# Optimization experiments

Measured on AMD Instinct MI355X. Metric: run time of the kernel, lower is better.

Reference implementation:

```python
import jax, jax.numpy as jnp
import numpy as np

NF, NLOC, NNEI = 4, 2048, 64
EMBED, PAIR_DIM, H = 128, 64, 8
HD = EMBED // H
EPS = 1e-5

def _ln(x, g, b):
    m = x.mean(-1, keepdims=True)
    v = ((x - m) ** 2).mean(-1, keepdims=True)
    return (x - m) * jax.lax.rsqrt(v + EPS) * g + b

def setup_inputs() -> dict:
    key = jax.random.key(0)
    ks = jax.random.split(key, 12)
    inp = {
        "query": jax.random.normal(ks[0], (NF, NLOC, EMBED), jnp.float32),
        "pair": jax.random.normal(ks[1], (NF, NLOC, NNEI, PAIR_DIM), jnp.float32),
        "nlist": jax.random.randint(ks[2], (NF, NLOC, NNEI), 0, NLOC, jnp.int64),
        "delta_pos": jax.random.normal(ks[3], (NF, NLOC, NNEI, 3), jnp.float32),
        "attn_mask": jnp.zeros((NF, H, NLOC, NNEI), jnp.float32),
        "ln_g": jnp.ones((EMBED,), jnp.float32),
        "ln_b": jnp.zeros((EMBED,), jnp.float32),
        "pn_g": jnp.ones((PAIR_DIM,), jnp.float32),
        "pn_b": jnp.zeros((PAIR_DIM,), jnp.float32),
        "Wq": jax.random.normal(ks[4], (EMBED, EMBED), jnp.float32) * (EMBED ** -0.5),
        "Wk": jax.random.normal(ks[5], (EMBED, EMBED), jnp.float32) * (EMBED ** -0.5),
        "Wv": jax.random.normal(ks[6], (EMBED, EMBED), jnp.float32) * (EMBED ** -0.5),
        "Wbias": jax.random.normal(ks[7], (H, PAIR_DIM), jnp.float32) * (PAIR_DIM ** -0.5),
        "bbias": jnp.zeros((H,), jnp.float32),
        "Wforce": jax.random.normal(ks[8], (1, EMBED), jnp.float32) * (EMBED ** -0.5),
    }
    return inp

def reference(query, pair, nlist, delta_pos, attn_mask,
              ln_g, ln_b, pn_g, pn_b, Wq, Wk, Wv, Wbias, bbias, Wforce):
    nf, nloc, _ = query.shape
    nnei = nlist.shape[-1]
    qn = _ln(query, ln_g, ln_b)            # [f,l,e]
    pn = _ln(pair, pn_g, pn_b)             # [f,l,n,p]
    scaling = HD ** -0.5
    q = (qn @ Wq.T).reshape(nf, nloc, H, HD) * scaling       # [f,l,h,d]
    k = qn @ Wk.T                                            # [f,l,e]
    v = qn @ Wv.T
    idx = nlist.reshape(nf, -1)[..., None]                   # [f,l*n,1]
    kg = jnp.take_along_axis(k, idx, axis=1).reshape(nf, nloc, nnei, H, HD)
    vg = jnp.take_along_axis(v, idx, axis=1).reshape(nf, nloc, nnei, H, HD)
    attn = jnp.einsum('flhd,flnhd->fhln', q, kg)             # [f,h,l,n]
    bias = jnp.einsum('flnp,hp->fhln', pn, Wbias) + bbias[None, :, None, None]
    probs = jax.nn.softmax(attn + attn_mask + bias, axis=-1)  # dropout off (eval)
    # rotate by delta_pos and contract with v over neighbors
    x = jnp.einsum('fhln,flnc,flnhd->flchd', probs, delta_pos, vg)
    x = x.reshape(nf, nloc, 3, EMBED)
    force = (x @ Wforce.T).squeeze(-1)                       # [f,l,3]
    return force
```

## Files before the change

### kernel.cpp

```cpp
#include <hip/hip_runtime.h>

#define NFR   4
#define NLOCC 2048
#define NNEIN 64
#define EMB   128
#define PDIM  64
#define NH    8
#define LNEPS 1e-5f
#define NROW  (NFR*NLOCC)

#define WS_Q   0
#define WS_K   (NROW*EMB)
#define WS_FV  (2*NROW*EMB)
#define WS_G   (2*NROW*EMB + NROW*NH)

__device__ __forceinline__ void fma4(float4& acc, const float4 a, const float4 b) {
    acc.x = fmaf(a.x, b.x, acc.x);
    acc.y = fmaf(a.y, b.y, acc.y);
    acc.z = fmaf(a.z, b.z, acc.z);
    acc.w = fmaf(a.w, b.w, acc.w);
}
__device__ __forceinline__ void fma4s(float4& acc, const float s, const float4 b) {
    acc.x = fmaf(s, b.x, acc.x);
    acc.y = fmaf(s, b.y, acc.y);
    acc.z = fmaf(s, b.z, acc.z);
    acc.w = fmaf(s, b.w, acc.w);
}
__device__ __forceinline__ float hsum4(const float4 a) {
    return (a.x + a.y) + (a.z + a.w);
}
__device__ __forceinline__ float dot4(const float4 a, const float4 b) {
    return fmaf(a.x, b.x, fmaf(a.y, b.y, fmaf(a.z, b.z, a.w * b.w)));
}
__device__ __forceinline__ float4 scale4(const float4 a, const float s) {
    return make_float4(a.x*s, a.y*s, a.z*s, a.w*s);
}

template<int CTRL>
__device__ __forceinline__ float dppf(float x) {
    return __int_as_float(__builtin_amdgcn_update_dpp(
        0, __float_as_int(x), CTRL, 0xF, 0xF, true));
}

__global__ __launch_bounds__(256, 2) void qkfv_kernel(
    const float* __restrict__ query,
    const float* __restrict__ ln_g, const float* __restrict__ ln_b,
    const float* __restrict__ Wq, const float* __restrict__ Wk,
    const float* __restrict__ Wv, const float* __restrict__ Wforce,
    const float* __restrict__ pn_g, const float* __restrict__ pn_b,
    const float* __restrict__ Wbias, const float* __restrict__ bbias,
    float* __restrict__ ws)
{
    __shared__ float  gb_s[2][EMB];
    __shared__ float  qn_s[16*132];
    __shared__ float  wt_s[2][16*132];
    __shared__ float4 wvf_s4[8*33];
    const int t = threadIdx.x;
    const int rowbase = blockIdx.x * 16;

    if (t < 64) {
        const float* src = (t < 32) ? ln_g : ln_b;
        ((float4*)gb_s[t >> 5])[t & 31] = ((const float4*)src)[t & 31];
    }

    if (blockIdx.x == 0) {
        if (t < 128) {
            const float4 wb4 = ((const float4*)Wbias)[t];
            const float4 pg4 = ((const float4*)pn_g)[t & 15];
            ((float4*)(ws + WS_G))[t] =
                make_float4(wb4.x*pg4.x, wb4.y*pg4.y, wb4.z*pg4.z, wb4.w*pg4.w);
        } else if (t < 192) {
            const int h = (t - 128) >> 3, s8 = (t - 128) & 7;
            float sg = 0.f, cb = 0.f;
            #pragma unroll
            for (int k = 0; k < 8; ++k) {
                const int p = s8*8 + k;
                const float wb = Wbias[h*PDIM + p];
                sg = fmaf(pn_g[p], wb, sg);
                cb = fmaf(pn_b[p], wb, cb);
            }
            sg += __shfl_xor(sg, 1, 64); sg += __shfl_xor(sg, 2, 64); sg += __shfl_xor(sg, 4, 64);
            cb += __shfl_xor(cb, 1, 64); cb += __shfl_xor(cb, 2, 64); cb += __shfl_xor(cb, 4, 64);
            if (s8 == 0) {
                ws[WS_G + 512 + h] = sg;
                ws[WS_G + 520 + h] = cb + bbias[h];
            }
        }
    }

    {
        const int h = t >> 5, ch = t & 31;
        float4 acc = make_float4(0.f, 0.f, 0.f, 0.f);
        #pragma unroll
        for (int d = 0; d < 16; ++d) {
            const float wf = Wforce[h*16 + d];
            const float4 wv = ((const float4*)(Wv + (size_t)(h*16 + d)*EMB))[ch];
            fma4s(acc, wf, wv);
        }
        wvf_s4[h*33 + ch] = acc;
    }

    const int r   = t >> 4;
    const int seg = t & 15;
    float4 x0 = ((const float4*)query)[(size_t)(rowbase + r)*32 + seg*2 + 0];
    float4 x1 = ((const float4*)query)[(size_t)(rowbase + r)*32 + seg*2 + 1];
    float s  = (x0.x + x0.y) + (x0.z + x0.w) + (x1.x + x1.y) + (x1.z + x1.w);
    float ss = x0.x*x0.x + x0.y*x0.y + x0.z*x0.z + x0.w*x0.w
             + x1.x*x1.x + x1.y*x1.y + x1.z*x1.z + x1.w*x1.w;
    #pragma unroll
    for (int m = 1; m < 16; m <<= 1) {
        s  += __shfl_xor(s,  m, 64);
        ss += __shfl_xor(ss, m, 64);
    }
    const float mean = s * (1.0f / 128.0f);
    const float var  = ss * (1.0f / 128.0f) - mean * mean;
    const float rstd = rsqrtf(var + LNEPS);
    __syncthreads();

    {
        const int c0 = seg * 8;
        float4 o0, o1;
        o0.x = (x0.x - mean)*rstd*gb_s[0][c0+0] + gb_s[1][c0+0];
        o0.y = (x0.y - mean)*rstd*gb_s[0][c0+1] + gb_s[1][c0+1];
        o0.z = (x0.z - mean)*rstd*gb_s[0][c0+2] + gb_s[1][c0+2];
        o0.w = (x0.w - mean)*rstd*gb_s[0][c0+3] + gb_s[1][c0+3];
        o1.x = (x1.x - mean)*rstd*gb_s[0][c0+4] + gb_s[1][c0+4];
        o1.y = (x1.y - mean)*rstd*gb_s[0][c0+5] + gb_s[1][c0+5];
        o1.z = (x1.z - mean)*rstd*gb_s[0][c0+6] + gb_s[1][c0+6];
        o1.w = (x1.w - mean)*rstd*gb_s[0][c0+7] + gb_s[1][c0+7];
        ((float4*)qn_s)[r*33 + seg*2 + 0] = o0;
        ((float4*)qn_s)[r*33 + seg*2 + 1] = o1;
    }
    __syncthreads();

    const int rp = t >> 5;
    const int r0 = rp * 2;
    const int cq = t & 31;
    const int sc0 = t >> 2;
    const int si0 = t & 3;
    const float4* qn4 = (const float4*)qn_s;

    for (int w = 0; w < 2; ++w) {
        const float4* W4 = (const float4*)((w == 0) ? Wq : Wk);
        float4 acc0 = make_float4(0.f,0.f,0.f,0.f);
        float4 acc1 = make_float4(0.f,0.f,0.f,0.f);
        {
            float4 g0 = W4[(size_t)sc0*32 + si0];
            float4 g1 = W4[(size_t)(sc0+64)*32 + si0];
            float* wt = wt_s[0];
            wt[(si0*4+0)*132 + sc0] = g0.x; wt[(si0*4+1)*132 + sc0] = g0.y;
            wt[(si0*4+2)*132 + sc0] = g0.z; wt[(si0*4+3)*132 + sc0] = g0.w;
            wt[(si0*4+0)*132 + sc0+64] = g1.x; wt[(si0*4+1)*132 + sc0+64] = g1.y;
            wt[(si0*4+2)*132 + sc0+64] = g1.z; wt[(si0*4+3)*132 + sc0+64] = g1.w;
        }
        __syncthreads();
        #pragma unroll
        for (int tau = 0; tau < 8; ++tau) {
            const int buf = tau & 1;
            float4 ng0, ng1;
            if (tau < 7) {
                ng0 = W4[(size_t)sc0*32 + (tau+1)*4 + si0];
                ng1 = W4[(size_t)(sc0+64)*32 + (tau+1)*4 + si0];
            }
            const float4* wt4 = (const float4*)wt_s[buf];
            #pragma unroll
            for (int e4 = 0; e4 < 4; ++e4) {
                float4 a0 = qn4[r0*33 + tau*4 + e4];
                float4 a1 = qn4[(r0+1)*33 + tau*4 + e4];
                const float* a0p = (const float*)&a0;
                const float* a1p = (const float*)&a1;
                #pragma unroll
                for (int ee = 0; ee < 4; ++ee) {
                    const float4 wv = wt4[(e4*4+ee)*33 + cq];
                    fma4s(acc0, a0p[ee], wv);
                    fma4s(acc1, a1p[ee], wv);
                }
            }
            if (tau < 7) {
                float* wt = wt_s[buf ^ 1];
                wt[(si0*4+0)*132 + sc0] = ng0.x; wt[(si0*4+1)*132 + sc0] = ng0.y;
                wt[(si0*4+2)*132 + sc0] = ng0.z; wt[(si0*4+3)*132 + sc0] = ng0.w;
                wt[(si0*4+0)*132 + sc0+64] = ng1.x; wt[(si0*4+1)*132 + sc0+64] = ng1.y;
                wt[(si0*4+2)*132 + sc0+64] = ng1.z; wt[(si0*4+3)*132 + sc0+64] = ng1.w;
            }
            __syncthreads();
        }
        const float sc = (w == 0) ? 0.25f : 1.0f;
        float4* dst = (float4*)(ws + (w == 0 ? WS_Q : WS_K));
        dst[(size_t)(rowbase + r0)*32 + cq]     = scale4(acc0, sc);
        dst[(size_t)(rowbase + r0 + 1)*32 + cq] = scale4(acc1, sc);
    }

    if (t < 128) {
        const int rr = t >> 3, h = t & 7;
        float4 acc = make_float4(0.f,0.f,0.f,0.f);
        #pragma unroll
        for (int ch = 0; ch < 32; ++ch)
            fma4(acc, qn4[rr*33 + ch], wvf_s4[h*33 + ch]);
        ws[WS_FV + (size_t)(rowbase + rr)*NH + h] = hsum4(acc);
    }
}

__global__ __launch_bounds__(256, 6) void attn_force_kernel(
    const float* __restrict__ pair, const int* __restrict__ nlist,
    const float* __restrict__ delta_pos, const float* __restrict__ attn_mask,
    const float* __restrict__ ws, float* __restrict__ out)
{
    __shared__ float  logit_s[NNEIN*9];
    __shared__ float  bias_s[NNEIN*9];
    __shared__ float  fv_s[NNEIN*9];
    __shared__ float  dp_s[192];
    __shared__ float4 gw_s4[4*128];
    __shared__ float  fpart[4][3];

    const int t    = threadIdx.x;
    const int bid  = blockIdx.x;
    const int fr   = bid >> 11;
    const int l    = bid & (NLOCC - 1);
    const int w    = t >> 6;
    const int lane = t & 63;
    const int n    = t >> 2;
    const int sub  = t & 3;
    const int half = lane >> 5;
    const int c    = lane & 31;
    const int hh   = t >> 5;
    const int i32  = lane & 31;

    int jr[8];
    #pragma unroll
    for (int i = 0; i < 8; ++i)
        jr[i] = nlist[(size_t)bid*NNEIN + ((w << 4) | (i << 1) | half)];
    const int jn = nlist[(size_t)bid*NNEIN + n];

    const float4 q4c = ((const float4*)(ws + WS_Q))[(size_t)bid*32 + c];

    const size_t mbase = (((size_t)(fr*NH + hh))*NLOCC + l)*NNEIN;
    const float ma = attn_mask[mbase + i32];
    const float mb = attn_mask[mbase + i32 + 32];

    const float4* pr4 = (const float4*)(pair + ((size_t)bid*NNEIN + n)*PDIM) + sub;
    const float4 p0 = pr4[0];
    const float4 p1 = pr4[4];
    const float4 p2 = pr4[8];
    const float4 p3 = pr4[12];

    {
        const float4* Gg = (const float4*)(ws + WS_G);
        gw_s4[(w << 7) | lane]        = Gg[lane];
        gw_s4[(w << 7) | (64 + lane)] = Gg[64 + lane];
    }

    if (t >= 192 && t < 240)
        ((float4*)dp_s)[t - 192] = ((const float4*)(delta_pos + (size_t)bid*192))[t - 192];

    const float4* k4 = (const float4*)(ws + WS_K) + (size_t)(fr << 11)*32;
    float4 kk[8];
    #pragma unroll
    for (int i = 0; i < 8; ++i) kk[i] = k4[(size_t)jr[i]*32 + c];

    {
        const float2 fv2 = ((const float2*)(ws + WS_FV + ((size_t)(fr << 11) + jn)*NH))[sub];
        fv_s[n*9 + sub*2]     = fv2.x;
        fv_s[n*9 + sub*2 + 1] = fv2.y;
    }

    {
        #pragma unroll
        for (int i = 0; i < 8; ++i) {
            float pp = dot4(kk[i], q4c);
            pp += dppf<0xB1>(pp);
            pp += dppf<0x4E>(pp);
            if ((c & 3) == 0)
                logit_s[((w << 4) | (i << 1) | half)*9 + (c >> 2)] = pp;
        }
    }

    {
        float s  = hsum4(p0) + hsum4(p1) + hsum4(p2) + hsum4(p3);
        float ss = dot4(p0,p0) + dot4(p1,p1) + dot4(p2,p2) + dot4(p3,p3);
        s  += dppf<0xB1>(s);  s  += dppf<0x4E>(s);
        ss += dppf<0xB1>(ss); ss += dppf<0x4E>(ss);

        float d[NH];
        #pragma unroll
        for (int h = 0; h < NH; ++h) d[h] = 0.f;
        const float4* gw = &gw_s4[w << 7];
        #pragma unroll
        for (int h = 0; h < NH; ++h) {
            d[h] += dot4(p0, gw[h*16 + 0*4 + sub]);
            d[h] += dot4(p1, gw[h*16 + 1*4 + sub]);
            d[h] += dot4(p2, gw[h*16 + 2*4 + sub]);
            d[h] += dot4(p3, gw[h*16 + 3*4 + sub]);
        }
        #pragma unroll
        for (int h = 0; h < NH; ++h) {
            d[h] += dppf<0xB1>(d[h]);
            d[h] += dppf<0x4E>(d[h]);
        }
        const float mean = s * (1.0f / 64.0f);
        const float var  = ss * (1.0f / 64.0f) - mean * mean;
        const float rstd = rsqrtf(var + LNEPS);
        const float* SGp = ws + WS_G + 512;
        const int h0 = sub*2, h1 = h0 + 1;
        bias_s[n*9 + h0] = rstd*(d[h0] - mean*SGp[h0]) + SGp[8 + h0];
        bias_s[n*9 + h1] = rstd*(d[h1] - mean*SGp[h1]) + SGp[8 + h1];
    }
    __syncthreads();

    {
        const float a = logit_s[i32*9 + hh]        + bias_s[i32*9 + hh]        + ma;
        const float b = logit_s[(i32 + 32)*9 + hh] + bias_s[(i32 + 32)*9 + hh] + mb;
        float m = fmaxf(a, b);
        m = fmaxf(m, __shfl_xor(m, 16, 64));
        m = fmaxf(m, __shfl_xor(m,  8, 64));
        m = fmaxf(m, __shfl_xor(m,  4, 64));
        m = fmaxf(m, dppf<0x4E>(m));
        m = fmaxf(m, dppf<0xB1>(m));
        const float ea = __expf(a - m), eb = __expf(b - m);
        float sum = ea + eb;
        sum += __shfl_xor(sum, 16, 64);
        sum += __shfl_xor(sum,  8, 64);
        sum += __shfl_xor(sum,  4, 64);
        sum += dppf<0x4E>(sum);
        sum += dppf<0xB1>(sum);
        const float inv = 1.0f / sum;
        const float ca = ea * inv * fv_s[i32*9 + hh];
        const float cb = eb * inv * fv_s[(i32 + 32)*9 + hh];

        const float dpax = dp_s[i32*3 + 0],      dpay = dp_s[i32*3 + 1],      dpaz = dp_s[i32*3 + 2];
        const float dpbx = dp_s[(i32+32)*3 + 0], dpby = dp_s[(i32+32)*3 + 1], dpbz = dp_s[(i32+32)*3 + 2];
        float f0 = ca*dpax + cb*dpbx;
        float f1 = ca*dpay + cb*dpby;
        float f2 = ca*dpaz + cb*dpbz;
        f0 += dppf<0x111>(f0); f0 += dppf<0x112>(f0); f0 += dppf<0x114>(f0); f0 += dppf<0x118>(f0);
        f0 += dppf<0x142>(f0); f0 += dppf<0x143>(f0);
        f1 += dppf<0x111>(f1); f1 += dppf<0x112>(f1); f1 += dppf<0x114>(f1); f1 += dppf<0x118>(f1);
        f1 += dppf<0x142>(f1); f1 += dppf<0x143>(f1);
        f2 += dppf<0x111>(f2); f2 += dppf<0x112>(f2); f2 += dppf<0x114>(f2); f2 += dppf<0x118>(f2);
        f2 += dppf<0x142>(f2); f2 += dppf<0x143>(f2);
        if (lane == 63) {
            fpart[w][0] = f0; fpart[w][1] = f1; fpart[w][2] = f2;
        }
    }
    __syncthreads();

    if (t < 3)
        out[(size_t)bid*3 + t] = fpart[0][t] + fpart[1][t] + fpart[2][t] + fpart[3][t];
}

extern "C" void kernel_launch(void* const* d_in, const int* in_sizes, int n_in,
                              void* d_out, int out_size, void* d_ws, size_t ws_size,
                              hipStream_t stream) {
    const float* query     = (const float*)d_in[0];
    const float* pair      = (const float*)d_in[1];
    const int*   nlist     = (const int*)d_in[2];
    const float* delta_pos = (const float*)d_in[3];
    const float* attn_mask = (const float*)d_in[4];
    const float* ln_g      = (const float*)d_in[5];
    const float* ln_b      = (const float*)d_in[6];
    const float* pn_g      = (const float*)d_in[7];
    const float* pn_b      = (const float*)d_in[8];
    const float* Wq        = (const float*)d_in[9];
    const float* Wk        = (const float*)d_in[10];
    const float* Wv        = (const float*)d_in[11];
    const float* Wbias     = (const float*)d_in[12];
    const float* bbias     = (const float*)d_in[13];
    const float* Wforce    = (const float*)d_in[14];
    float* out = (float*)d_out;
    float* ws  = (float*)d_ws;

    qkfv_kernel<<<512, 256, 0, stream>>>(query, ln_g, ln_b, Wq, Wk, Wv, Wforce,
                                         pn_g, pn_b, Wbias, bbias, ws);
    attn_force_kernel<<<NROW, 256, 0, stream>>>(pair, nlist, delta_pos, attn_mask,
                                                ws, out);
}
```

Before: 254.0 us.

## Move pair-bias LayerNorm projection into first kernel as extra blocks

The pair LayerNorm and bias projection move out of the attention kernel into 2048 extra blocks of the first kernel. Each of those blocks processes four rows and writes an [h,n] bias tensor to workspace, and the attention kernel reads that tensor directly. This shortens the attention kernel and lowers its shared-memory use, which can raise occupancy. It also lets the bias work run alongside the QKV projection blocks. The cost is an extra workspace round-trip of NROW*512 floats, and the first kernel now streams the full pair tensor.

```diff
diff --git a/kernel.cpp b/kernel.cpp
--- a/kernel.cpp
+++ b/kernel.cpp
@@ -9,10 +9,10 @@
 #define LNEPS 1e-5f
 #define NROW  (NFR*NLOCC)
 
-#define WS_Q   0
-#define WS_K   (NROW*EMB)
-#define WS_FV  (2*NROW*EMB)
-#define WS_G   (2*NROW*EMB + NROW*NH)
+#define WS_Q    0
+#define WS_K    (NROW*EMB)
+#define WS_FV   (2*NROW*EMB)
+#define WS_BIAS (2*NROW*EMB + NROW*NH)
 
 __device__ __forceinline__ void fma4(float4& acc, const float4 a, const float4 b) {
     acc.x = fmaf(a.x, b.x, acc.x);
@@ -42,8 +42,8 @@
         0, __float_as_int(x), CTRL, 0xF, 0xF, true));
 }
 
-__global__ __launch_bounds__(256, 2) void qkfv_kernel(
-    const float* __restrict__ query,
+__global__ __launch_bounds__(256, 2) void qkfv_bias_kernel(
+    const float* __restrict__ query, const float* __restrict__ pair,
     const float* __restrict__ ln_g, const float* __restrict__ ln_b,
     const float* __restrict__ Wq, const float* __restrict__ Wk,
     const float* __restrict__ Wv, const float* __restrict__ Wforce,
@@ -56,19 +56,18 @@
     __shared__ float  wt_s[2][16*132];
     __shared__ float4 wvf_s4[8*33];
     const int t = threadIdx.x;
-    const int rowbase = blockIdx.x * 16;
-
-    if (t < 64) {
-        const float* src = (t < 32) ? ln_g : ln_b;
-        ((float4*)gb_s[t >> 5])[t & 31] = ((const float4*)src)[t & 31];
-    }
-
-    if (blockIdx.x == 0) {
+
+    if (blockIdx.x >= 512) {
+        float4* gw4   = wvf_s4;
+        float*  csg   = (float*)gb_s;
+        float*  out_s = qn_s;
+        const int row0 = (blockIdx.x - 512) << 2;
+        const int n = t >> 2, sub = t & 3;
+
         if (t < 128) {
             const float4 wb4 = ((const float4*)Wbias)[t];
             const float4 pg4 = ((const float4*)pn_g)[t & 15];
-            ((float4*)(ws + WS_G))[t] =
-                make_float4(wb4.x*pg4.x, wb4.y*pg4.y, wb4.z*pg4.z, wb4.w*pg4.w);
+            gw4[t] = make_float4(wb4.x*pg4.x, wb4.y*pg4.y, wb4.z*pg4.z, wb4.w*pg4.w);
         } else if (t < 192) {
             const int h = (t - 128) >> 3, s8 = (t - 128) & 7;
             float sg = 0.f, cb = 0.f;
@@ -81,11 +80,57 @@
             }
             sg += __shfl_xor(sg, 1, 64); sg += __shfl_xor(sg, 2, 64); sg += __shfl_xor(sg, 4, 64);
             cb += __shfl_xor(cb, 1, 64); cb += __shfl_xor(cb, 2, 64); cb += __shfl_xor(cb, 4, 64);
-            if (s8 == 0) {
-                ws[WS_G + 512 + h] = sg;
-                ws[WS_G + 520 + h] = cb + bbias[h];
-            }
-        }
+            if (s8 == 0) { csg[h] = sg; csg[8 + h] = cb + bbias[h]; }
+        }
+        __syncthreads();
+
+        #pragma unroll
+        for (int r = 0; r < 4; ++r) {
+            const float4* pr4 = (const float4*)(pair + ((size_t)(row0 + r)*NNEIN + n)*PDIM) + sub;
+            const float4 p0 = pr4[0];
+            const float4 p1 = pr4[4];
+            const float4 p2 = pr4[8];
+            const float4 p3 = pr4[12];
+            float s  = hsum4(p0) + hsum4(p1) + hsum4(p2) + hsum4(p3);
+            float ss = dot4(p0,p0) + dot4(p1,p1) + dot4(p2,p2) + dot4(p3,p3);
+            s  += dppf<0xB1>(s);  s  += dppf<0x4E>(s);
+            ss += dppf<0xB1>(ss); ss += dppf<0x4E>(ss);
+
+            float d[NH];
+            #pragma unroll
+            for (int h = 0; h < NH; ++h) d[h] = 0.f;
+            #pragma unroll
+            for (int h = 0; h < NH; ++h) {
+                d[h] += dot4(p0, gw4[h*16 + 0*4 + sub]);
+                d[h] += dot4(p1, gw4[h*16 + 1*4 + sub]);
+                d[h] += dot4(p2, gw4[h*16 + 2*4 + sub]);
+                d[h] += dot4(p3, gw4[h*16 + 3*4 + sub]);
+            }
+            #pragma unroll
+            for (int h = 0; h < NH; ++h) {
+                d[h] += dppf<0xB1>(d[h]);
+                d[h] += dppf<0x4E>(d[h]);
+            }
+            const float mean = s * (1.0f / 64.0f);
+            const float var  = ss * (1.0f / 64.0f) - mean * mean;
+            const float rstd = rsqrtf(var + LNEPS);
+            const int h0 = sub*2, h1 = h0 + 1;
+            out_s[r*512 + h0*64 + n] = rstd*(d[h0] - mean*csg[h0]) + csg[8 + h0];
+            out_s[r*512 + h1*64 + n] = rstd*(d[h1] - mean*csg[h1]) + csg[8 + h1];
+        }
+        __syncthreads();
+
+        float4* dst = (float4*)(ws + WS_BIAS + (size_t)row0*512);
+        dst[t*2]     = ((const float4*)out_s)[t*2];
+        dst[t*2 + 1] = ((const float4*)out_s)[t*2 + 1];
+        return;
+    }
+
+    const int rowbase = blockIdx.x * 16;
+
+    if (t < 64) {
+        const float* src = (t < 32) ? ln_g : ln_b;
+        ((float4*)gb_s[t >> 5])[t & 31] = ((const float4*)src)[t & 31];
     }
 
     {
@@ -202,16 +247,14 @@
 }
 
 __global__ __launch_bounds__(256, 6) void attn_force_kernel(
-    const float* __restrict__ pair, const int* __restrict__ nlist,
+    const int* __restrict__ nlist,
     const float* __restrict__ delta_pos, const float* __restrict__ attn_mask,
     const float* __restrict__ ws, float* __restrict__ out)
 {
-    __shared__ float  logit_s[NNEIN*9];
-    __shared__ float  bias_s[NNEIN*9];
-    __shared__ float  fv_s[NNEIN*9];
-    __shared__ float  dp_s[192];
-    __shared__ float4 gw_s4[4*128];
-    __shared__ float  fpart[4][3];
+    __shared__ float logit_s[NNEIN*9];
+    __shared__ float fv_s[NNEIN*9];
+    __shared__ float dp_s[192];
+    __shared__ float fpart[4][3];
 
     const int t    = threadIdx.x;
     const int bid  = blockIdx.x;
@@ -238,17 +281,9 @@
     const float ma = attn_mask[mbase + i32];
     const float mb = attn_mask[mbase + i32 + 32];
 
-    const float4* pr4 = (const float4*)(pair + ((size_t)bid*NNEIN + n)*PDIM) + sub;
-    const float4 p0 = pr4[0];
-    const float4 p1 = pr4[4];
-    const float4 p2 = pr4[8];
-    const float4 p3 = pr4[12];
-
-    {
-        const float4* Gg = (const float4*)(ws + WS_G);
-        gw_s4[(w << 7) | lane]        = Gg[lane];
-        gw_s4[(w << 7) | (64 + lane)] = Gg[64 + lane];
-    }
+    const float* bbase = ws + WS_BIAS + (size_t)bid*512 + hh*64;
+    const float ba = bbase[i32];
+    const float bb = bbase[i32 + 32];
 
     if (t >= 192 && t < 240)
         ((float4*)dp_s)[t - 192] = ((const float4*)(delta_pos + (size_t)bid*192))[t - 192];
@@ -264,52 +299,19 @@
         fv_s[n*9 + sub*2 + 1] = fv2.y;
     }
 
+    #pragma unroll
+    for (int i = 0; i < 8; ++i) {
+        float pp = dot4(kk[i], q4c);
+        pp += dppf<0xB1>(pp);
+        pp += dppf<0x4E>(pp);
+        if ((c & 3) == 0)
+            logit_s[((w << 4) | (i << 1) | half)*9 + (c >> 2)] = pp;
+    }
+    __syncthreads();
+
     {
-        #pragma unroll
-        for (int i = 0; i < 8; ++i) {
-            float pp = dot4(kk[i], q4c);
-            pp += dppf<0xB1>(pp);
-            pp += dppf<0x4E>(pp);
-            if ((c & 3) == 0)
-                logit_s[((w << 4) | (i << 1) | half)*9 + (c >> 2)] = pp;
-        }
-    }
-
-    {
-        float s  = hsum4(p0) + hsum4(p1) + hsum4(p2) + hsum4(p3);
-        float ss = dot4(p0,p0) + dot4(p1,p1) + dot4(p2,p2) + dot4(p3,p3);
-        s  += dppf<0xB1>(s);  s  += dppf<0x4E>(s);
-        ss += dppf<0xB1>(ss); ss += dppf<0x4E>(ss);
-
-        float d[NH];
-        #pragma unroll
-        for (int h = 0; h < NH; ++h) d[h] = 0.f;
-        const float4* gw = &gw_s4[w << 7];
-        #pragma unroll
-        for (int h = 0; h < NH; ++h) {
-            d[h] += dot4(p0, gw[h*16 + 0*4 + sub]);
-            d[h] += dot4(p1, gw[h*16 + 1*4 + sub]);
-            d[h] += dot4(p2, gw[h*16 + 2*4 + sub]);
-            d[h] += dot4(p3, gw[h*16 + 3*4 + sub]);
-        }
-        #pragma unroll
-        for (int h = 0; h < NH; ++h) {
-            d[h] += dppf<0xB1>(d[h]);
-            d[h] += dppf<0x4E>(d[h]);
-        }
-        const float mean = s * (1.0f / 64.0f);
-        const float var  = ss * (1.0f / 64.0f) - mean * mean;
-        const float rstd = rsqrtf(var + LNEPS);
-        const float* SGp = ws + WS_G + 512;
-        const int h0 = sub*2, h1 = h0 + 1;
-        bias_s[n*9 + h0] = rstd*(d[h0] - mean*SGp[h0]) + SGp[8 + h0];
-        bias_s[n*9 + h1] = rstd*(d[h1] - mean*SGp[h1]) + SGp[8 + h1];
-    }
-    __syncthreads();
-
-    {
-        const float a = logit_s[i32*9 + hh]        + bias_s[i32*9 + hh]        + ma;
-        const float b = logit_s[(i32 + 32)*9 + hh] + bias_s[(i32 + 32)*9 + hh] + mb;
+        const float a = logit_s[i32*9 + hh]        + ba + ma;
+        const float b = logit_s[(i32 + 32)*9 + hh] + bb + mb;
         float m = fmaxf(a, b);
         m = fmaxf(m, __shfl_xor(m, 16, 64));
         m = fmaxf(m, __shfl_xor(m,  8, 64));
@@ -369,8 +371,9 @@
     float* out = (float*)d_out;
     float* ws  = (float*)d_ws;
 
-    qkfv_kernel<<<512, 256, 0, stream>>>(query, ln_g, ln_b, Wq, Wk, Wv, Wforce,
-                                         pn_g, pn_b, Wbias, bbias, ws);
-    attn_force_kernel<<<NROW, 256, 0, stream>>>(pair, nlist, delta_pos, attn_mask,
+    qkfv_bias_kernel<<<2560, 256, 0, stream>>>(query, pair, ln_g, ln_b, Wq, Wk,
+                                               Wv, Wforce, pn_g, pn_b, Wbias,
+                                               bbias, ws);
+    attn_force_kernel<<<NROW, 256, 0, stream>>>(nlist, delta_pos, attn_mask,
                                                 ws, out);
 }
```

Result: slower. 333.3 us (+31.2%).
